# Performance work log

Measured on AMD Instinct MI355X. Metric: run time of the kernel, lower is better.

The kernel has to match this reference:

```python
import jax, jax.numpy as jnp
import numpy as np

EPS = 1e-5
QMAX = 127.0

def setup_inputs() -> dict:
    key = jax.random.key(0)
    k_x, k_w = jax.random.split(key)
    B, S, DIN, DOUT = 8, 2048, 4096, 4096
    x = jax.random.normal(k_x, (B, S, DIN), dtype=jnp.float32)
    # Learned full-precision weight (kaiming-normal, fan_out) then ternarized,
    # mimicking BitLinear._post_init -> terniarize(params).
    std = np.sqrt(2.0 / DOUT)
    w_fp = jax.random.normal(k_w, (DOUT, DIN), dtype=jnp.float32) * std
    scale_w = 1.0 / jnp.clip(jnp.mean(jnp.abs(w_fp)), 1e-5)   # scalar, matches terniarize
    w_ternary = jnp.clip(jnp.round(w_fp * scale_w), -1.0, 1.0)  # values in {-1,0,1}, stored as f32
    gamma = jnp.ones((DIN,), dtype=jnp.float32)                 # RMSNorm weight
    bias = jnp.zeros((DOUT,), dtype=jnp.float32)                # init.constant_(bias, 0)
    return {"x": x, "w_ternary": w_ternary, "scale_w": scale_w, "gamma": gamma, "bias": bias}

def reference(x, w_ternary, scale_w, gamma, bias):
    # 1) RMSNorm over last dim (in_features)
    var = jnp.mean(jnp.square(x), axis=-1, keepdims=True)
    xn = x * jax.lax.rsqrt(var + EPS) * gamma
    # 2) bitmat: per-token absmax int8 quantization of activations
    scale_x = QMAX / jnp.clip(jnp.max(jnp.abs(xn), axis=-1, keepdims=True), 1e-5)  # [B,S,1]
    xq = jnp.clip(jnp.round(xn * scale_x), -128.0, 127.0)
    # 3) ternary matmul (int math expressed in f32) + inline dequant by scale_x*scale_w
    acc = jnp.einsum('bsk,ok->bso', xq, w_ternary)  # [B,S,DOUT]
    out = acc / (scale_x * scale_w)
    # 4) bias
    return out + bias
```

## Files before the change

kernel.cpp:

```cpp
#include <hip/hip_runtime.h>
#include <cstdint>

#define DIN 4096
#define DOUT 4096
#define QMAXF 127.0f

typedef int v4i __attribute__((ext_vector_type(4)));
typedef unsigned int u32;

__device__ __forceinline__ void async16(const void* g, void* l) {
  __builtin_amdgcn_global_load_lds((const __attribute__((address_space(1))) u32*)g,
                                   (__attribute__((address_space(3))) u32*)l,
                                   16, 0, 0);
}

__device__ __forceinline__ int clamp_q(float v) {
  int i = (int)rintf(v);
  return i < -128 ? -128 : (i > 127 ? 127 : i);
}

__global__ __launch_bounds__(256) void wconvert_kernel(const float* __restrict__ w,
                                                       int8_t* __restrict__ wq) {
  int t = blockIdx.x * 256 + threadIdx.x;
  float4 v = ((const float4*)w)[t];
  int b0 = ((int)v.x) & 255, b1 = ((int)v.y) & 255;
  int b2 = ((int)v.z) & 255, b3 = ((int)v.w) & 255;
  ((int*)wq)[t] = b0 | (b1 << 8) | (b2 << 16) | (b3 << 24);
}

__global__ __launch_bounds__(256) void rmsnorm_quant_kernel(
    const float* __restrict__ x, const float* __restrict__ gamma,
    const float* __restrict__ scale_w_ptr, int8_t* __restrict__ xq,
    float* __restrict__ inv_scale) {
  const int token = blockIdx.x;
  const float* xr = x + (size_t)token * DIN;
  const int t = threadIdx.x;

  float4 xv[4], gv[4];
  float ss = 0.f, amax = 0.f;
#pragma unroll
  for (int i = 0; i < 4; ++i) {
    const int idx = (i * 256 + t) * 4;
    xv[i] = *(const float4*)(xr + idx);
    gv[i] = *(const float4*)(gamma + idx);
    ss += xv[i].x * xv[i].x + xv[i].y * xv[i].y + xv[i].z * xv[i].z + xv[i].w * xv[i].w;
    amax = fmaxf(amax, fabsf(xv[i].x * gv[i].x));
    amax = fmaxf(amax, fabsf(xv[i].y * gv[i].y));
    amax = fmaxf(amax, fabsf(xv[i].z * gv[i].z));
    amax = fmaxf(amax, fabsf(xv[i].w * gv[i].w));
  }
#pragma unroll
  for (int o = 32; o > 0; o >>= 1) {
    ss += __shfl_down(ss, o);
    amax = fmaxf(amax, __shfl_down(amax, o));
  }
  __shared__ float s_ss[4], s_am[4];
  const int wave = t >> 6, lane = t & 63;
  if (lane == 0) { s_ss[wave] = ss; s_am[wave] = amax; }
  __syncthreads();
  const float tot = s_ss[0] + s_ss[1] + s_ss[2] + s_ss[3];
  const float mx = fmaxf(fmaxf(s_am[0], s_am[1]), fmaxf(s_am[2], s_am[3]));
  const float rstd = rsqrtf(tot * (1.0f / DIN) + 1e-5f);
  const float absmax = fmaxf(mx * rstd, 1e-5f);
  const float qscale = rstd * (QMAXF / absmax);
  if (t == 0) inv_scale[token] = absmax / (QMAXF * scale_w_ptr[0]);

  int* qr = (int*)(xq + (size_t)token * DIN);
#pragma unroll
  for (int i = 0; i < 4; ++i) {
    const int idx4 = i * 256 + t;
    int b0 = clamp_q(xv[i].x * gv[i].x * qscale) & 255;
    int b1 = clamp_q(xv[i].y * gv[i].y * qscale) & 255;
    int b2 = clamp_q(xv[i].z * gv[i].z * qscale) & 255;
    int b3 = clamp_q(xv[i].w * gv[i].w * qscale) & 255;
    qr[idx4] = b0 | (b1 << 8) | (b2 << 16) | (b3 << 24);
  }
}

#define BT 256
#define BK 64

__global__ __launch_bounds__(512, 2) void gemm_i8_kernel(
    const int8_t* __restrict__ xq, const int8_t* __restrict__ wq,
    const float* __restrict__ inv_scale, const float* __restrict__ bias,
    float* __restrict__ out) {
  __shared__ __align__(16) int8_t As[4][BT * BK];
  __shared__ __align__(16) int8_t Bs[4][BT * BK];

  const int t = threadIdx.x;
  const int wave = t >> 6, lane = t & 63;
  const int m0 = blockIdx.y * BT, n0 = blockIdx.x * BT;
  const int wm = wave >> 2;
  const int wn = wave & 3;
  const int fr = lane & 15, q = lane >> 4;

  int srow[2], scol[2];
#pragma unroll
  for (int i = 0; i < 2; ++i) {
    const int p = i * 512 + t;
    srow[i] = p >> 2;
    scol[i] = (((p & 3) - (srow[i] >> 1)) & 3) * 16;
  }

  const int8_t* Ag = xq + (size_t)m0 * DIN;
  const int8_t* Bg = wq + (size_t)n0 * DIN;

  const int swz = ((q + (fr >> 1)) & 3) * 16;
  int offA[8], offB[4];
#pragma unroll
  for (int mi = 0; mi < 8; ++mi) offA[mi] = (wm * 128 + mi * 16 + fr) * BK + swz;
#pragma unroll
  for (int ni = 0; ni < 4; ++ni) offB[ni] = (wn * 64 + ni * 16 + fr) * BK + swz;

  v4i acc[8][4];
#pragma unroll
  for (int mi = 0; mi < 8; ++mi)
#pragma unroll
    for (int ni = 0; ni < 4; ++ni) acc[mi][ni] = (v4i){0, 0, 0, 0};

#define STAGE_A(buf, kt)                                                        \
  do {                                                                          \
    async16(Ag + (size_t)srow[0] * DIN + (kt) * BK + scol[0], &As[buf][t * 16]);\
    async16(Ag + (size_t)srow[1] * DIN + (kt) * BK + scol[1],                   \
            &As[buf][8192 + t * 16]);                                           \
  } while (0)
#define STAGE_B(buf, kt)                                                        \
  do {                                                                          \
    async16(Bg + (size_t)srow[0] * DIN + (kt) * BK + scol[0], &Bs[buf][t * 16]);\
    async16(Bg + (size_t)srow[1] * DIN + (kt) * BK + scol[1],                   \
            &Bs[buf][8192 + t * 16]);                                           \
  } while (0)

#define VMCNT8 asm volatile("s_waitcnt vmcnt(8)" ::: "memory")
#define VMCNT4 asm volatile("s_waitcnt vmcnt(4)" ::: "memory")
#define VMCNT0 asm volatile("s_waitcnt vmcnt(0)" ::: "memory")

#define KTILE(bufidx, DO_STAGE, kt, WAITSTMT)                                   \
  do {                                                                          \
    const int8_t* Ab = &As[bufidx][0];                                          \
    const int8_t* Bb = &Bs[bufidx][0];                                          \
    v4i a[4], b[4];                                                             \
    _Pragma("unroll") for (int j = 0; j < 4; ++j)                               \
        b[j] = *(const v4i*)(Bb + offB[j]);                                     \
    _Pragma("unroll") for (int j = 0; j < 4; ++j)                               \
        a[j] = *(const v4i*)(Ab + offA[j]);                                     \
    if (DO_STAGE) STAGE_A(((kt) + 3) & 3, (kt) + 3);                            \
    __builtin_amdgcn_s_barrier();                                               \
    __builtin_amdgcn_s_setprio(1);                                              \
    _Pragma("unroll") for (int mi = 0; mi < 4; ++mi)                            \
        _Pragma("unroll") for (int ni = 0; ni < 4; ++ni)                        \
            acc[mi][ni] = __builtin_amdgcn_mfma_i32_16x16x64_i8(                \
                a[mi], b[ni], acc[mi][ni], 0, 0, 0);                            \
    __builtin_amdgcn_s_setprio(0);                                              \
    __builtin_amdgcn_s_barrier();                                               \
    _Pragma("unroll") for (int j = 0; j < 4; ++j)                               \
        a[j] = *(const v4i*)(Ab + offA[4 + j]);                                 \
    if (DO_STAGE) STAGE_B(((kt) + 3) & 3, (kt) + 3);                            \
    __builtin_amdgcn_s_barrier();                                               \
    __builtin_amdgcn_s_setprio(1);                                              \
    _Pragma("unroll") for (int mi = 0; mi < 4; ++mi)                            \
        _Pragma("unroll") for (int ni = 0; ni < 4; ++ni)                        \
            acc[4 + mi][ni] = __builtin_amdgcn_mfma_i32_16x16x64_i8(            \
                a[mi], b[ni], acc[4 + mi][ni], 0, 0, 0);                        \
    __builtin_amdgcn_s_setprio(0);                                              \
    WAITSTMT;                                                                   \
    __builtin_amdgcn_s_barrier();                                               \
  } while (0)

  STAGE_A(0, 0); STAGE_B(0, 0);
  STAGE_A(1, 1); STAGE_B(1, 1);
  STAGE_A(2, 2); STAGE_B(2, 2);
  VMCNT8;
  __builtin_amdgcn_s_barrier();

  const int NT = DIN / BK;
#pragma unroll 1
  for (int kt = 0; kt < NT - 3; ++kt)
    KTILE(kt & 3, true, kt, VMCNT8);
  KTILE(1, false, 0, VMCNT4);
  KTILE(2, false, 0, VMCNT0);
  KTILE(3, false, 0, (void)0);

  const int col = lane & 15;
  const int rb = (lane >> 4) * 4;
#pragma unroll
  for (int mi = 0; mi < 8; ++mi) {
    float sc[4];
#pragma unroll
    for (int r = 0; r < 4; ++r) sc[r] = inv_scale[m0 + wm * 128 + mi * 16 + rb + r];
#pragma unroll
    for (int ni = 0; ni < 4; ++ni) {
      const int gc = n0 + wn * 64 + ni * 16 + col;
      const float bb = bias[gc];
#pragma unroll
      for (int r = 0; r < 4; ++r) {
        const int gr = m0 + wm * 128 + mi * 16 + rb + r;
        out[(size_t)gr * DOUT + gc] = (float)acc[mi][ni][r] * sc[r] + bb;
      }
    }
  }
}

extern "C" void kernel_launch(void* const* d_in, const int* in_sizes, int n_in,
                              void* d_out, int out_size, void* d_ws, size_t ws_size,
                              hipStream_t stream) {
  const float* x       = (const float*)d_in[0];
  const float* w       = (const float*)d_in[1];
  const float* scale_w = (const float*)d_in[2];
  const float* gamma   = (const float*)d_in[3];
  const float* bias    = (const float*)d_in[4];
  float* out = (float*)d_out;
  const int M = in_sizes[0] / DIN;

  int8_t* wq = (int8_t*)d_ws;
  int8_t* xq = wq + (size_t)DOUT * DIN;
  float* inv_scale = (float*)(xq + (size_t)M * DIN);

  hipLaunchKernelGGL(wconvert_kernel, dim3((DOUT * DIN) / (256 * 4)), dim3(256), 0, stream,
                     w, wq);
  hipLaunchKernelGGL(rmsnorm_quant_kernel, dim3(M), dim3(256), 0, stream,
                     x, gamma, scale_w, xq, inv_scale);
  hipLaunchKernelGGL(gemm_i8_kernel, dim3(DOUT / BT, M / BT), dim3(512), 0, stream,
                     xq, wq, inv_scale, bias, out);
}
```

Measured before the change: 788.6 us.

## Double-buffer LDS fragment reads in int8 GEMM and persist rmsnorm blocks

The GEMM main loop is rebuilt so that register fragments for the next K tile are read from LDS while the MFMAs for the current tile run, using two register sets (a0/b0, a1/b1). This drops from three barriers per K tile to one, and A and B staging are merged into a single issue point. The rmsnorm/quant kernel becomes grid-stride with 2048 blocks and loads gamma once per block instead of once per token. The cost is much higher register pressure from holding two full fragment sets next to the 32 accumulators, which could cause spills or lower occupancy under launch_bounds(512,2).

Result: no change. 783.9 us (-0.6%).

```diff
diff --git a/kernel.cpp b/kernel.cpp
--- a/kernel.cpp
+++ b/kernel.cpp
@@ -31,49 +31,53 @@
 __global__ __launch_bounds__(256) void rmsnorm_quant_kernel(
     const float* __restrict__ x, const float* __restrict__ gamma,
     const float* __restrict__ scale_w_ptr, int8_t* __restrict__ xq,
-    float* __restrict__ inv_scale) {
-  const int token = blockIdx.x;
-  const float* xr = x + (size_t)token * DIN;
+    float* __restrict__ inv_scale, int M) {
   const int t = threadIdx.x;
-
-  float4 xv[4], gv[4];
-  float ss = 0.f, amax = 0.f;
-#pragma unroll
-  for (int i = 0; i < 4; ++i) {
-    const int idx = (i * 256 + t) * 4;
-    xv[i] = *(const float4*)(xr + idx);
-    gv[i] = *(const float4*)(gamma + idx);
-    ss += xv[i].x * xv[i].x + xv[i].y * xv[i].y + xv[i].z * xv[i].z + xv[i].w * xv[i].w;
-    amax = fmaxf(amax, fabsf(xv[i].x * gv[i].x));
-    amax = fmaxf(amax, fabsf(xv[i].y * gv[i].y));
-    amax = fmaxf(amax, fabsf(xv[i].z * gv[i].z));
-    amax = fmaxf(amax, fabsf(xv[i].w * gv[i].w));
-  }
-#pragma unroll
-  for (int o = 32; o > 0; o >>= 1) {
-    ss += __shfl_down(ss, o);
-    amax = fmaxf(amax, __shfl_down(amax, o));
-  }
+  const int wave = t >> 6, lane = t & 63;
   __shared__ float s_ss[4], s_am[4];
-  const int wave = t >> 6, lane = t & 63;
-  if (lane == 0) { s_ss[wave] = ss; s_am[wave] = amax; }
-  __syncthreads();
-  const float tot = s_ss[0] + s_ss[1] + s_ss[2] + s_ss[3];
-  const float mx = fmaxf(fmaxf(s_am[0], s_am[1]), fmaxf(s_am[2], s_am[3]));
-  const float rstd = rsqrtf(tot * (1.0f / DIN) + 1e-5f);
-  const float absmax = fmaxf(mx * rstd, 1e-5f);
-  const float qscale = rstd * (QMAXF / absmax);
-  if (t == 0) inv_scale[token] = absmax / (QMAXF * scale_w_ptr[0]);
-
-  int* qr = (int*)(xq + (size_t)token * DIN);
-#pragma unroll
-  for (int i = 0; i < 4; ++i) {
-    const int idx4 = i * 256 + t;
-    int b0 = clamp_q(xv[i].x * gv[i].x * qscale) & 255;
-    int b1 = clamp_q(xv[i].y * gv[i].y * qscale) & 255;
-    int b2 = clamp_q(xv[i].z * gv[i].z * qscale) & 255;
-    int b3 = clamp_q(xv[i].w * gv[i].w * qscale) & 255;
-    qr[idx4] = b0 | (b1 << 8) | (b2 << 16) | (b3 << 24);
+
+  float4 gv[4];
+#pragma unroll
+  for (int i = 0; i < 4; ++i) gv[i] = *(const float4*)(gamma + (i * 256 + t) * 4);
+  const float sw = scale_w_ptr[0];
+
+  for (int token = blockIdx.x; token < M; token += gridDim.x) {
+    const float* xr = x + (size_t)token * DIN;
+    float4 xv[4];
+    float ss = 0.f, amax = 0.f;
+#pragma unroll
+    for (int i = 0; i < 4; ++i) {
+      xv[i] = *(const float4*)(xr + (i * 256 + t) * 4);
+      ss += xv[i].x * xv[i].x + xv[i].y * xv[i].y + xv[i].z * xv[i].z + xv[i].w * xv[i].w;
+      amax = fmaxf(amax, fabsf(xv[i].x * gv[i].x));
+      amax = fmaxf(amax, fabsf(xv[i].y * gv[i].y));
+      amax = fmaxf(amax, fabsf(xv[i].z * gv[i].z));
+      amax = fmaxf(amax, fabsf(xv[i].w * gv[i].w));
+    }
+#pragma unroll
+    for (int o = 32; o > 0; o >>= 1) {
+      ss += __shfl_down(ss, o);
+      amax = fmaxf(amax, __shfl_down(amax, o));
+    }
+    if (lane == 0) { s_ss[wave] = ss; s_am[wave] = amax; }
+    __syncthreads();
+    const float tot = s_ss[0] + s_ss[1] + s_ss[2] + s_ss[3];
+    const float mx = fmaxf(fmaxf(s_am[0], s_am[1]), fmaxf(s_am[2], s_am[3]));
+    const float rstd = rsqrtf(tot * (1.0f / DIN) + 1e-5f);
+    const float absmax = fmaxf(mx * rstd, 1e-5f);
+    const float qscale = rstd * (QMAXF / absmax);
+    if (t == 0) inv_scale[token] = absmax / (QMAXF * sw);
+
+    int* qr = (int*)(xq + (size_t)token * DIN);
+#pragma unroll
+    for (int i = 0; i < 4; ++i) {
+      int b0 = clamp_q(xv[i].x * gv[i].x * qscale) & 255;
+      int b1 = clamp_q(xv[i].y * gv[i].y * qscale) & 255;
+      int b2 = clamp_q(xv[i].z * gv[i].z * qscale) & 255;
+      int b3 = clamp_q(xv[i].w * gv[i].w * qscale) & 255;
+      qr[i * 256 + t] = b0 | (b1 << 8) | (b2 << 16) | (b3 << 24);
+    }
+    __syncthreads();
   }
 }
 
@@ -118,68 +122,68 @@
 #pragma unroll
     for (int ni = 0; ni < 4; ++ni) acc[mi][ni] = (v4i){0, 0, 0, 0};
 
-#define STAGE_A(buf, kt)                                                        \
+#define STAGE_AB(buf, kt)                                                       \
   do {                                                                          \
     async16(Ag + (size_t)srow[0] * DIN + (kt) * BK + scol[0], &As[buf][t * 16]);\
     async16(Ag + (size_t)srow[1] * DIN + (kt) * BK + scol[1],                   \
             &As[buf][8192 + t * 16]);                                           \
-  } while (0)
-#define STAGE_B(buf, kt)                                                        \
-  do {                                                                          \
     async16(Bg + (size_t)srow[0] * DIN + (kt) * BK + scol[0], &Bs[buf][t * 16]);\
     async16(Bg + (size_t)srow[1] * DIN + (kt) * BK + scol[1],                   \
             &Bs[buf][8192 + t * 16]);                                           \
   } while (0)
 
-#define VMCNT8 asm volatile("s_waitcnt vmcnt(8)" ::: "memory")
+#define READF(A_, B_, bufi)                                                     \
+  do {                                                                          \
+    const int8_t* Ab_ = &As[bufi][0];                                           \
+    const int8_t* Bb_ = &Bs[bufi][0];                                           \
+    _Pragma("unroll") for (int j = 0; j < 4; ++j)                               \
+        B_[j] = *(const v4i*)(Bb_ + offB[j]);                                   \
+    _Pragma("unroll") for (int j = 0; j < 8; ++j)                               \
+        A_[j] = *(const v4i*)(Ab_ + offA[j]);                                   \
+  } while (0)
+
+#define MMA(A_, B_)                                                             \
+  do {                                                                          \
+    __builtin_amdgcn_s_setprio(1);                                              \
+    _Pragma("unroll") for (int mi = 0; mi < 8; ++mi)                            \
+        _Pragma("unroll") for (int ni = 0; ni < 4; ++ni)                        \
+            acc[mi][ni] = __builtin_amdgcn_mfma_i32_16x16x64_i8(                \
+                A_[mi], B_[ni], acc[mi][ni], 0, 0, 0);                          \
+    __builtin_amdgcn_s_setprio(0);                                              \
+  } while (0)
+
 #define VMCNT4 asm volatile("s_waitcnt vmcnt(4)" ::: "memory")
 #define VMCNT0 asm volatile("s_waitcnt vmcnt(0)" ::: "memory")
-
-#define KTILE(bufidx, DO_STAGE, kt, WAITSTMT)                                   \
-  do {                                                                          \
-    const int8_t* Ab = &As[bufidx][0];                                          \
-    const int8_t* Bb = &Bs[bufidx][0];                                          \
-    v4i a[4], b[4];                                                             \
-    _Pragma("unroll") for (int j = 0; j < 4; ++j)                               \
-        b[j] = *(const v4i*)(Bb + offB[j]);                                     \
-    _Pragma("unroll") for (int j = 0; j < 4; ++j)                               \
-        a[j] = *(const v4i*)(Ab + offA[j]);                                     \
-    if (DO_STAGE) STAGE_A(((kt) + 3) & 3, (kt) + 3);                            \
+#define MEMFENCE asm volatile("" ::: "memory")
+
+#define KT(CA, CB, NA, NB, kt, DO_STAGE, WAIT)                                  \
+  do {                                                                          \
+    if (DO_STAGE) STAGE_AB(((kt) + 3) & 3, (kt) + 3);                           \
+    READF(NA, NB, ((kt) + 1) & 3);                                              \
+    MMA(CA, CB);                                                                \
+    WAIT;                                                                       \
     __builtin_amdgcn_s_barrier();                                               \
-    __builtin_amdgcn_s_setprio(1);                                              \
-    _Pragma("unroll") for (int mi = 0; mi < 4; ++mi)                            \
-        _Pragma("unroll") for (int ni = 0; ni < 4; ++ni)                        \
-            acc[mi][ni] = __builtin_amdgcn_mfma_i32_16x16x64_i8(                \
-                a[mi], b[ni], acc[mi][ni], 0, 0, 0);                            \
-    __builtin_amdgcn_s_setprio(0);                                              \
-    __builtin_amdgcn_s_barrier();                                               \
-    _Pragma("unroll") for (int j = 0; j < 4; ++j)                               \
-        a[j] = *(const v4i*)(Ab + offA[4 + j]);                                 \
-    if (DO_STAGE) STAGE_B(((kt) + 3) & 3, (kt) + 3);                            \
-    __builtin_amdgcn_s_barrier();                                               \
-    __builtin_amdgcn_s_setprio(1);                                              \
-    _Pragma("unroll") for (int mi = 0; mi < 4; ++mi)                            \
-        _Pragma("unroll") for (int ni = 0; ni < 4; ++ni)                        \
-            acc[4 + mi][ni] = __builtin_amdgcn_mfma_i32_16x16x64_i8(            \
-                a[mi], b[ni], acc[4 + mi][ni], 0, 0, 0);                        \
-    __builtin_amdgcn_s_setprio(0);                                              \
-    WAITSTMT;                                                                   \
-    __builtin_amdgcn_s_barrier();                                               \
-  } while (0)
-
-  STAGE_A(0, 0); STAGE_B(0, 0);
-  STAGE_A(1, 1); STAGE_B(1, 1);
-  STAGE_A(2, 2); STAGE_B(2, 2);
-  VMCNT8;
+  } while (0)
+
+  STAGE_AB(0, 0);
+  STAGE_AB(1, 1);
+  STAGE_AB(2, 2);
+  VMCNT4;
   __builtin_amdgcn_s_barrier();
+
+  v4i a0[8], b0[4], a1[8], b1[4];
+  READF(a0, b0, 0);
 
   const int NT = DIN / BK;
 #pragma unroll 1
-  for (int kt = 0; kt < NT - 3; ++kt)
-    KTILE(kt & 3, true, kt, VMCNT8);
-  KTILE(1, false, 0, VMCNT4);
-  KTILE(2, false, 0, VMCNT0);
-  KTILE(3, false, 0, (void)0);
+  for (int kt = 0; kt < NT - 4; kt += 2) {
+    KT(a0, b0, a1, b1, kt,     true, VMCNT4);
+    KT(a1, b1, a0, b0, kt + 1, true, VMCNT4);
+  }
+  KT(a0, b0, a1, b1, 60, true,  VMCNT4);
+  KT(a1, b1, a0, b0, 61, false, VMCNT0);
+  KT(a0, b0, a1, b1, 62, false, MEMFENCE);
+  MMA(a1, b1);
 
   const int col = lane & 15;
   const int rb = (lane >> 4) * 4;
@@ -218,8 +222,8 @@
 
   hipLaunchKernelGGL(wconvert_kernel, dim3((DOUT * DIN) / (256 * 4)), dim3(256), 0, stream,
                      w, wq);
-  hipLaunchKernelGGL(rmsnorm_quant_kernel, dim3(M), dim3(256), 0, stream,
-                     x, gamma, scale_w, xq, inv_scale);
+  hipLaunchKernelGGL(rmsnorm_quant_kernel, dim3(2048), dim3(256), 0, stream,
+                     x, gamma, scale_w, xq, inv_scale, M);
   hipLaunchKernelGGL(gemm_i8_kernel, dim3(DOUT / BT, M / BT), dim3(512), 0, stream,
                      xq, wq, inv_scale, bias, out);
 }
```
